# Kernel optimization log

Measured on AMD Instinct MI355X. Metric: run time of the kernel, lower is better.

The kernel has to match this reference:

```python
import jax, jax.numpy as jnp
import numpy as np

NEG = -1e9  # sentinel for suppressed / below-threshold scores
SCORE_THRESHOLD = 0.05
IOU_THRESHOLD = 0.5
MAX_DETECTIONS = 100


def _iou_one_vs_all(box, boxes):
    # box: (4,) in (x1, y1, x2, y2); boxes: (N, 4)
    ix1 = jnp.maximum(box[0], boxes[:, 0])
    iy1 = jnp.maximum(box[1], boxes[:, 1])
    ix2 = jnp.minimum(box[2], boxes[:, 2])
    iy2 = jnp.minimum(box[3], boxes[:, 3])
    inter = jnp.maximum(ix2 - ix1, 0.0) * jnp.maximum(iy2 - iy1, 0.0)
    a1 = (box[2] - box[0]) * (box[3] - box[1])
    a2 = (boxes[:, 2] - boxes[:, 0]) * (boxes[:, 3] - boxes[:, 1])
    return inter / jnp.maximum(a1 + a2 - inter, 1e-8)


def _nms_single_class(boxes, scores):
    # boxes: (N, 4), scores: (N,). Fixed-shape greedy NMS via scan.
    scores0 = jnp.where(scores > SCORE_THRESHOLD, scores, NEG)

    def step(s, _):
        best = jnp.argmax(s)
        bscore = s[best]
        bbox = boxes[best]
        iou = _iou_one_vs_all(bbox, boxes)
        # suppress overlapping boxes (incl. the selected one, IoU=1)
        s_next = jnp.where(iou > IOU_THRESHOLD, NEG, s)
        return s_next, (bscore, bbox)

    _, (keep_scores, keep_boxes) = jax.lax.scan(step, scores0, None, length=MAX_DETECTIONS)
    return keep_scores, keep_boxes  # (M,), (M, 4)


def _filter_one_image(boxes, classification):
    # boxes: (N, 4), classification: (N, C)
    C = classification.shape[1]
    cls_scores = classification.T  # (C, N)
    ks, kb = jax.vmap(lambda s: _nms_single_class(boxes, s))(cls_scores)  # (C, M), (C, M, 4)
    labels = jnp.broadcast_to(jnp.arange(C, dtype=jnp.int32)[:, None], ks.shape)
    scores_flat = ks.reshape(-1)          # (C*M,)
    boxes_flat = kb.reshape(-1, 4)        # (C*M, 4)
    labels_flat = labels.reshape(-1)      # (C*M,)
    top_scores, top_idx = jax.lax.top_k(scores_flat, MAX_DETECTIONS)
    top_boxes = boxes_flat[top_idx]
    top_labels = labels_flat[top_idx]
    valid = top_scores > SCORE_THRESHOLD
    out_scores = jnp.where(valid, top_scores, -1.0)
    out_boxes = jnp.where(valid[:, None], top_boxes, -1.0)
    out_labels = jnp.where(valid, top_labels, -1).astype(jnp.int32)
    return out_boxes, out_scores, out_labels


def setup_inputs() -> dict:
    key = jax.random.key(0)
    k1, k2, k3 = jax.random.split(key, 3)
    B, N, C = 2, 10000, 80
    xy = jax.random.uniform(k1, (B, N, 2), dtype=jnp.float32) * 900.0
    wh = jax.random.uniform(k2, (B, N, 2), dtype=jnp.float32) * 100.0 + 1.0
    boxes = jnp.concatenate([xy, xy + wh], axis=-1)  # valid (x1,y1,x2,y2)
    # raise to 4th power so most scores fall below the 0.05 threshold (realistic)
    classification = jax.random.uniform(k3, (B, N, C), dtype=jnp.float32) ** 4
    return {"boxes": boxes, "classification": classification}


@jax.jit
def reference(boxes, classification):
    # boxes: (B, N, 4), classification: (B, N, C)
    out_boxes, out_scores, out_labels = jax.vmap(_filter_one_image)(boxes, classification)
    return out_boxes, out_scores, out_labels
```

## Files before the change

kernel.cpp:

```cpp
#include <hip/hip_runtime.h>
#include <float.h>
#include <stdint.h>

#pragma clang fp contract(off)

#define NEGV   (-1e9f)
#define THRV   (0.05f)
#define MAXDET 100
#define NB     1152
#define BKBASE 31385
#define SLABSZ 1024
#define CHTGT  512
#define TKCAP  1024

__device__ __forceinline__ int bktOf(unsigned u) {
  int v = (int)(u >> 15) - BKBASE;
  return v < 0 ? 0 : (v > NB - 1 ? NB - 1 : v);
}

__device__ __forceinline__ bool killpair(
    float qx1, float qy1, float qx2, float qy2, float qa,
    float x1, float y1, float x2, float y2, float a)
{
  const float iw = fminf(qx2, x2) - fmaxf(qx1, x1);
  const float ih = fminf(qy2, y2) - fmaxf(qy1, y1);
  if (iw <= 0.f || ih <= 0.f) return false;
  const float inter = iw * ih;
  const float den = fmaxf((qa + a) - inter, 1e-8f);
  const float i2 = inter + inter;
  if (i2 > den * 1.00001f) return true;
  if (i2 < den * 0.99999f) return false;
  return (inter / den) > 0.5f;
}

template<int BT>
__device__ __forceinline__ int suffix_scan(int* hist, int* wtot,
                                           int tid, int lane, int wid) {
  int c0 = 0, c1 = 0, c2 = 0;
  if (tid < NB / 3) {
    c0 = hist[NB - 1 - 3 * tid];
    c1 = hist[NB - 2 - 3 * tid];
    c2 = hist[NB - 3 - 3 * tid];
  }
  const int tsum = c0 + c1 + c2;
  int inc = tsum;
#pragma unroll
  for (int off = 1; off < 64; off <<= 1) {
    const int u = __shfl_up(inc, off, 64);
    if (lane >= off) inc += u;
  }
  if (lane == 63) wtot[wid] = inc;
  __syncthreads();
  int wbase = 0, tot = 0;
#pragma unroll
  for (int w = 0; w < BT / 64; ++w) {
    const int v = wtot[w];
    if (w < wid) wbase += v;
    tot += v;
  }
  const int excl = wbase + inc - tsum;
  if (tid < NB / 3) {
    hist[NB - 1 - 3 * tid] = excl;
    hist[NB - 2 - 3 * tid] = excl + c0;
    hist[NB - 3 - 3 * tid] = excl + c0 + c1;
  }
  __syncthreads();
  return tot;
}

template<int BT>
__device__ int run_scan(
    const unsigned long long* kL, const unsigned long long* kG, bool useL,
    int cn, const float4* __restrict__ bb4,
    float4* kboxS, float* kscoreS, float* kareaS,
    unsigned long long* wkill, unsigned long long* killby,
    int tid, int lane, int wid)
{
#pragma clang fp contract(off)
  constexpr int NW = BT / 64;
  constexpr int CPW = 64 / NW;
  int nk = 0;
  for (int base = 0; base < cn && nk < MAXDET; base += 64) {
    const int nc = min(64, cn - base);
    const bool valid = lane < nc;
    const int p = base + lane;
    unsigned long long key = 0ull;
    if (valid) key = useL ? kL[p] : kG[p];
    const float score = __uint_as_float((unsigned)(key >> 32));
    const int idx = (int)(~(unsigned)key);
    float4 bx = make_float4(0.f, 0.f, 0.f, 0.f);
    if (valid) bx = bb4[idx];
    const float area = (bx.z - bx.x) * (bx.w - bx.y);

    bool kill = false;
    for (int e = wid; e < nk; e += NW) {
      const float4 q = kboxS[e];
      kill = kill || killpair(q.x, q.y, q.z, q.w, kareaS[e],
                              bx.x, bx.y, bx.z, bx.w, area);
    }
    {
      const unsigned long long bm = __ballot(valid && kill);
      if (lane == 0) wkill[wid] = bm;
    }
    {
      const int cb = wid * CPW;
#pragma unroll
      for (int jj = 0; jj < CPW; ++jj) {
        const int j = cb + jj;
        if (j < nc) {
          const float jx1 = __int_as_float(__builtin_amdgcn_readlane(__float_as_int(bx.x), j));
          const float jy1 = __int_as_float(__builtin_amdgcn_readlane(__float_as_int(bx.y), j));
          const float jx2 = __int_as_float(__builtin_amdgcn_readlane(__float_as_int(bx.z), j));
          const float jy2 = __int_as_float(__builtin_amdgcn_readlane(__float_as_int(bx.w), j));
          const float ja  = __int_as_float(__builtin_amdgcn_readlane(__float_as_int(area), j));
          const bool kij = valid && killpair(jx1, jy1, jx2, jy2, ja,
                                             bx.x, bx.y, bx.z, bx.w, area);
          const unsigned long long bm = __ballot(kij);
          if (lane == 0) killby[j] = bm;
        }
      }
    }
    __syncthreads();

    unsigned long long kmask = 0;
#pragma unroll
    for (int w = 0; w < NW; ++w) kmask |= wkill[w];
    unsigned long long alive = ~kmask;
    alive &= (nc >= 64) ? ~0ull : ((1ull << nc) - 1ull);
    const unsigned long long kb = killby[lane];
    for (int j = 0; j < 64; ++j) {
      if ((alive >> j) & 1ull) {
        const unsigned klo = (unsigned)__builtin_amdgcn_readlane((int)(unsigned)kb, j);
        const unsigned khi = (unsigned)__builtin_amdgcn_readlane((int)(unsigned)(kb >> 32), j);
        const unsigned long long km = ((unsigned long long)khi << 32) | klo;
        alive &= ~(km & ((~1ull) << j));
      }
    }
    if (wid == 0) {
      const int rank = (int)__popcll(alive & ((1ull << lane) - 1ull));
      if (((alive >> lane) & 1ull) && (nk + rank < MAXDET)) {
        kboxS[nk + rank] = bx;
        kscoreS[nk + rank] = score;
        kareaS[nk + rank] = area;
      }
    }
    nk += min((int)__popcll(alive), MAXDET - nk);
    __syncthreads();
  }
  return nk;
}

__global__ __launch_bounds__(256, 1) void transpose_kernel(
    const float* __restrict__ cls, float* __restrict__ clsT, int N, int C)
{
  __shared__ float tile[32][33];
  const int b = blockIdx.z;
  const int n0 = blockIdx.x * 32, c0 = blockIdx.y * 32;
  const int tx = threadIdx.x, ty = threadIdx.y;
#pragma unroll
  for (int r = ty; r < 32; r += 8) {
    const int n = n0 + r, c = c0 + tx;
    if (n < N && c < C) tile[r][tx] = cls[((size_t)b * N + n) * C + c];
  }
  __syncthreads();
#pragma unroll
  for (int r = ty; r < 32; r += 8) {
    const int c = c0 + r, n = n0 + tx;
    if (n < N && c < C) clsT[((size_t)b * C + c) * N + n] = tile[tx][r];
  }
}

template<int BT>
__global__ __launch_bounds__(BT, 1) void nms_kernel(
    const float* __restrict__ boxes, const float* __restrict__ clsT,
    unsigned long long* __restrict__ skg_all,
    float* __restrict__ ksc, float* __restrict__ kbx,
    int* __restrict__ ihist, int N, int C)
{
#pragma clang fp contract(off)
  const int bc = blockIdx.x;
  const int tid = threadIdx.x, lane = tid & 63, wid = tid >> 6;

  const float* ct = clsT + (size_t)bc * N;
  const float4* bb4 = (const float4*)(boxes + (size_t)(bc / C) * N * 4);
  unsigned long long* skg = skg_all + (size_t)bc * N;

  __shared__ unsigned long long slab[SLABSZ];
  __shared__ unsigned long long sorted[SLABSZ];
  __shared__ int hist[NB];
  __shared__ int wtot[BT / 64];
  __shared__ float4 kboxS[MAXDET];
  __shared__ float  kscoreS[MAXDET];
  __shared__ float  kareaS[MAXDET];
  __shared__ unsigned long long wkill[BT / 64];
  __shared__ unsigned long long killby[64];
  __shared__ int bkLoS;

  for (int i = tid; i < NB; i += BT) hist[i] = 0;
  if (tid == 0) bkLoS = -1;
  __syncthreads();
  for (int i = tid; i < N; i += BT) {
    const float s = ct[i];
    if (s > THRV) atomicAdd(&hist[bktOf(__float_as_uint(s))], 1);
  }
  __syncthreads();

  const int cn = suffix_scan<BT>(hist, wtot, tid, lane, wid);

  for (int bk = tid; bk < NB; bk += BT)
    if (hist[bk] >= CHTGT) atomicMax(&bkLoS, bk);
  __syncthreads();
  const int bkLo = bkLoS;
  const int chunkCnt = (bkLo >= 0) ? hist[bkLo] : cn;

  int nk = 0;
  bool slow = (chunkCnt > SLABSZ);
  if (!slow) {
    for (int i = tid; i < N; i += BT) {
      const float s = ct[i];
      if (s > THRV) {
        const unsigned u = __float_as_uint(s);
        const int bk = bktOf(u);
        if (bk > bkLo) {
          const int pos = atomicAdd(&hist[bk], 1);
          slab[pos] = ((unsigned long long)u << 32) | (unsigned)(~i);
        }
      }
    }
    __syncthreads();
    for (int e = tid; e < chunkCnt; e += BT) {
      const unsigned long long k = slab[e];
      int r = 0;
      for (int j = 0; j < chunkCnt; ++j) r += (slab[j] > k) ? 1 : 0;
      sorted[r] = k;
    }
    __syncthreads();
    nk = run_scan<BT>(sorted, skg, true, chunkCnt, bb4,
                      kboxS, kscoreS, kareaS, wkill, killby, tid, lane, wid);
    slow = (nk < MAXDET && chunkCnt < cn);
  }

  if (slow) {
    __syncthreads();
    for (int i = tid; i < NB; i += BT) hist[i] = 0;
    __syncthreads();
    for (int i = tid; i < N; i += BT) {
      const float s = ct[i];
      if (s > THRV) atomicAdd(&hist[bktOf(__float_as_uint(s))], 1);
    }
    __syncthreads();
    suffix_scan<BT>(hist, wtot, tid, lane, wid);
    for (int i = tid; i < N; i += BT) {
      const float s = ct[i];
      if (s > THRV) {
        const unsigned u = __float_as_uint(s);
        const int pos = atomicAdd(&hist[bktOf(u)], 1);
        skg[pos] = ((unsigned long long)u << 32) | (unsigned)(~i);
      }
    }
    __syncthreads();
    for (int bk = tid; bk < NB; bk += BT) {
      const int lo = (bk == NB - 1) ? 0 : hist[bk + 1];
      const int hi = hist[bk];
      for (int x = lo + 1; x < hi; ++x) {
        const unsigned long long v = skg[x];
        int y = x - 1;
        while (y >= lo && skg[y] < v) { skg[y + 1] = skg[y]; --y; }
        skg[y + 1] = v;
      }
    }
    __syncthreads();
    nk = run_scan<BT>(sorted, skg, false, cn, bb4,
                      kboxS, kscoreS, kareaS, wkill, killby, tid, lane, wid);
  }

  float* ko  = ksc + (size_t)bc * MAXDET;
  float* kbo = kbx + (size_t)bc * MAXDET * 4;
  int* ih = ihist + (size_t)(bc / C) * NB;
  for (int e = tid; e < MAXDET; e += BT) {
    if (e < nk) {
      const float4 q = kboxS[e];
      const float s = kscoreS[e];
      ko[e] = s;
      kbo[e * 4 + 0] = q.x; kbo[e * 4 + 1] = q.y;
      kbo[e * 4 + 2] = q.z; kbo[e * 4 + 3] = q.w;
      atomicAdd(&ih[bktOf(__float_as_uint(s))], 1);
    } else {
      ko[e] = NEGV;
      kbo[e * 4 + 0] = 0.f; kbo[e * 4 + 1] = 0.f;
      kbo[e * 4 + 2] = 0.f; kbo[e * 4 + 3] = 0.f;
    }
  }
}

template<int BT>
__global__ __launch_bounds__(BT, 1) void topk_kernel(
    const float* __restrict__ ksc, const float* __restrict__ kbx,
    const int* __restrict__ ihist, unsigned long long* __restrict__ gcand_all,
    float* __restrict__ out, int B, int C)
{
  const int b = blockIdx.x;
  const int tid = threadIdx.x, lane = tid & 63, wid = tid >> 6;
  const int T = C * MAXDET;
  const float* s0 = ksc + (size_t)b * T;
  unsigned long long* gc = gcand_all + (size_t)b * T;
  float* ob = out;
  float* os = out + (size_t)B * MAXDET * 4;
  float* ol = os + (size_t)B * MAXDET;

  __shared__ int hist[NB];
  __shared__ int wtot[BT / 64];
  __shared__ unsigned long long cand[TKCAP];
  __shared__ int tBs, cposS;

  for (int i = tid; i < NB; i += BT) hist[i] = ihist[(size_t)b * NB + i];
  if (tid == 0) { cposS = 0; tBs = 0; }
  __syncthreads();
  suffix_scan<BT>(hist, wtot, tid, lane, wid);
  for (int bk = tid; bk < NB; bk += BT)
    if (hist[bk] < MAXDET && (bk == 0 || hist[bk - 1] >= MAXDET)) tBs = bk;
  __syncthreads();
  const int t = tBs;
  for (int f = tid; f < T; f += BT) {
    const float s = s0[f];
    if (s > THRV) {
      const unsigned u = __float_as_uint(s);
      if (bktOf(u) >= t) {
        const int p = atomicAdd(&cposS, 1);
        const unsigned long long key =
            ((unsigned long long)u << 32) | (unsigned)(~f);
        if (p < TKCAP) cand[p] = key; else gc[p] = key;
      }
    }
  }
  __syncthreads();
  const int nc = cposS;
  const int nw = min(nc, MAXDET);
  for (int s2 = nw + tid; s2 < MAXDET; s2 += BT) {
    float* od = ob + ((size_t)b * MAXDET + s2) * 4;
    od[0] = -1.f; od[1] = -1.f; od[2] = -1.f; od[3] = -1.f;
    os[(size_t)b * MAXDET + s2] = -1.f;
    ol[(size_t)b * MAXDET + s2] = -1.f;
  }
  for (int e = tid; e < nc; e += BT) {
    const unsigned long long k = (e < TKCAP) ? cand[e] : gc[e];
    int rank = 0;
    for (int j = 0; j < nc; ++j) {
      const unsigned long long o = (j < TKCAP) ? cand[j] : gc[j];
      rank += (o > k) ? 1 : 0;
    }
    if (rank < MAXDET) {
      const int f = (int)(~(unsigned)k);
      const float sc = __uint_as_float((unsigned)(k >> 32));
      const float* bp = kbx + ((size_t)b * T + f) * 4;
      float* od = ob + ((size_t)b * MAXDET + rank) * 4;
      od[0] = bp[0]; od[1] = bp[1]; od[2] = bp[2]; od[3] = bp[3];
      os[(size_t)b * MAXDET + rank] = sc;
      ol[(size_t)b * MAXDET + rank] = (float)(f / MAXDET);
    }
  }
}

extern "C" void kernel_launch(void* const* d_in, const int* in_sizes, int n_in,
                              void* d_out, int out_size, void* d_ws, size_t ws_size,
                              hipStream_t stream) {
  const float* boxes = (const float*)d_in[0];
  const float* cls   = (const float*)d_in[1];
  const int B = out_size / (MAXDET * 6);
  const int N = in_sizes[0] / (B * 4);
  const int C = in_sizes[1] / (B * N);

  char* ws = (char*)d_ws;
  unsigned long long* skg = (unsigned long long*)ws;
  ws += (size_t)B * C * N * 8;
  unsigned long long* gcand = (unsigned long long*)ws;
  ws += (size_t)B * C * MAXDET * 8;
  float* clsT = (float*)ws; ws += (size_t)B * C * N * 4;
  float* kbx = (float*)ws;  ws += (size_t)B * C * MAXDET * 16;
  float* ksc = (float*)ws;  ws += (size_t)B * C * MAXDET * 4;
  int* ihist = (int*)ws;

  hipMemsetAsync(ihist, 0, (size_t)B * NB * 4, stream);
  transpose_kernel<<<dim3((N + 31) / 32, (C + 31) / 32, B), dim3(32, 8),
                     0, stream>>>(cls, clsT, N, C);
  nms_kernel<1024><<<dim3(B * C), dim3(1024), 0, stream>>>(
      boxes, clsT, skg, ksc, kbx, ihist, N, C);
  topk_kernel<1024><<<dim3(B), dim3(1024), 0, stream>>>(
      ksc, kbx, ihist, gcand, (float*)d_out, B, C);
}
```

Before: 159.6 us.

## Fuse threshold compaction and histogram into transpose sweep, replace slow path with selection

```diff
diff --git a/kernel.cpp b/kernel.cpp
--- a/kernel.cpp
+++ b/kernel.cpp
@@ -11,6 +11,7 @@
 #define BKBASE 31385
 #define SLABSZ 1024
 #define CHTGT  512
+#define PREB   256
 #define TKCAP  1024
 
 __device__ __forceinline__ int bktOf(unsigned u) {
@@ -69,12 +70,12 @@
 }
 
 template<int BT>
-__device__ int run_scan(
-    const unsigned long long* kL, const unsigned long long* kG, bool useL,
-    int cn, const float4* __restrict__ bb4,
-    float4* kboxS, float* kscoreS, float* kareaS,
-    unsigned long long* wkill, unsigned long long* killby,
-    int tid, int lane, int wid)
+__device__ int run_scan(const unsigned long long* keys, int cn,
+                        const float4* __restrict__ bb4,
+                        const float4* boxPre, int preN,
+                        float4* kboxS, float* kscoreS, float* kareaS,
+                        unsigned long long* wkill, unsigned long long* killby,
+                        int tid, int lane, int wid)
 {
 #pragma clang fp contract(off)
   constexpr int NW = BT / 64;
@@ -85,11 +86,11 @@
     const bool valid = lane < nc;
     const int p = base + lane;
     unsigned long long key = 0ull;
-    if (valid) key = useL ? kL[p] : kG[p];
+    if (valid) key = keys[p];
     const float score = __uint_as_float((unsigned)(key >> 32));
     const int idx = (int)(~(unsigned)key);
     float4 bx = make_float4(0.f, 0.f, 0.f, 0.f);
-    if (valid) bx = bb4[idx];
+    if (valid) bx = (p < preN) ? boxPre[p] : bb4[idx];
     const float area = (bx.z - bx.x) * (bx.w - bx.y);
 
     bool kill = false;
@@ -150,63 +151,130 @@
   return nk;
 }
 
-__global__ __launch_bounds__(256, 1) void transpose_kernel(
-    const float* __restrict__ cls, float* __restrict__ clsT, int N, int C)
+template<int BT>
+__device__ int selection_tail(const unsigned long long* __restrict__ cd,
+                              int cn, unsigned long long lastKey, int nk,
+                              const float4* __restrict__ bb4,
+                              float4* kboxS, float* kscoreS, float* kareaS,
+                              unsigned long long* redS, int* flagS,
+                              int tid, int lane, int wid)
+{
+#pragma clang fp contract(off)
+  while (nk < MAXDET) {
+    unsigned long long best = 0ull;
+    for (int i = tid; i < cn; i += BT) {
+      const unsigned long long k = cd[i];
+      if (k < lastKey && k > best) best = k;
+    }
+#pragma unroll
+    for (int off = 32; off >= 1; off >>= 1) {
+      const unsigned long long o = __shfl_xor(best, off, 64);
+      if (o > best) best = o;
+    }
+    if (lane == 0) redS[wid] = best;
+    if (tid == 0) *flagS = 0;
+    __syncthreads();
+    unsigned long long gbest = redS[0];
+#pragma unroll
+    for (int w = 1; w < BT / 64; ++w) if (redS[w] > gbest) gbest = redS[w];
+    if (gbest == 0ull) break;
+    const int idx = (int)(~(unsigned)gbest);
+    const float4 q = bb4[idx];
+    const float qa = (q.z - q.x) * (q.w - q.y);
+    bool kl = false;
+    for (int e = tid; e < nk; e += BT) {
+      const float4 kq = kboxS[e];
+      kl = kl || killpair(kq.x, kq.y, kq.z, kq.w, kareaS[e],
+                          q.x, q.y, q.z, q.w, qa);
+    }
+    if (kl) atomicOr(flagS, 1);
+    __syncthreads();
+    const bool killed = (*flagS != 0);
+    if (!killed) {
+      if (tid == 0) {
+        kboxS[nk] = q;
+        kscoreS[nk] = __uint_as_float((unsigned)(gbest >> 32));
+        kareaS[nk] = qa;
+      }
+      ++nk;
+    }
+    __syncthreads();
+    lastKey = gbest;
+  }
+  return nk;
+}
+
+__global__ __launch_bounds__(256, 1) void sweep_kernel(
+    const float* __restrict__ cls, unsigned long long* __restrict__ cand,
+    int* __restrict__ cnt, int* __restrict__ ghist, int N, int C)
 {
   __shared__ float tile[32][33];
   const int b = blockIdx.z;
   const int n0 = blockIdx.x * 32, c0 = blockIdx.y * 32;
   const int tx = threadIdx.x, ty = threadIdx.y;
-#pragma unroll
   for (int r = ty; r < 32; r += 8) {
     const int n = n0 + r, c = c0 + tx;
     if (n < N && c < C) tile[r][tx] = cls[((size_t)b * N + n) * C + c];
   }
   __syncthreads();
-#pragma unroll
-  for (int r = ty; r < 32; r += 8) {
-    const int c = c0 + r, n = n0 + tx;
-    if (n < N && c < C) clsT[((size_t)b * C + c) * N + n] = tile[tx][r];
+  const int t = ty * 32 + tx;
+  const int l = t & 31;
+  const int g = t >> 5;
+  const int lane = t & 63;
+#pragma unroll
+  for (int pass = 0; pass < 4; ++pass) {
+    const int ccol = pass * 8 + g;
+    const int c = c0 + ccol;
+    const int n = n0 + l;
+    const float s = tile[l][ccol];
+    const bool pred = (c < C) && (n < N) && (s > THRV);
+    const unsigned long long bal = __ballot(pred);
+    const unsigned hm = (unsigned)(bal >> (lane & 32));
+    const int npass = __popc(hm);
+    int base = 0;
+    if ((l == 0) && npass) base = atomicAdd(&cnt[b * C + c], npass);
+    base = __shfl(base, lane & 32, 64);
+    if (pred) {
+      const unsigned u = __float_as_uint(s);
+      const int rank = __popc(hm & ((1u << l) - 1u));
+      const size_t bcIdx = (size_t)(b * C + c);
+      cand[bcIdx * N + base + rank] =
+          ((unsigned long long)u << 32) | (unsigned)(~n);
+      atomicAdd(&ghist[bcIdx * NB + bktOf(u)], 1);
+    }
   }
 }
 
 template<int BT>
 __global__ __launch_bounds__(BT, 1) void nms_kernel(
-    const float* __restrict__ boxes, const float* __restrict__ clsT,
-    unsigned long long* __restrict__ skg_all,
-    float* __restrict__ ksc, float* __restrict__ kbx,
-    int* __restrict__ ihist, int N, int C)
+    const float* __restrict__ boxes,
+    const unsigned long long* __restrict__ cand,
+    const int* __restrict__ cnt, const int* __restrict__ ghist,
+    float* __restrict__ ksc, float* __restrict__ kbx, int N, int C)
 {
 #pragma clang fp contract(off)
   const int bc = blockIdx.x;
+  const int cn = cnt[bc];
   const int tid = threadIdx.x, lane = tid & 63, wid = tid >> 6;
-
-  const float* ct = clsT + (size_t)bc * N;
+  const unsigned long long* cd = cand + (size_t)bc * N;
   const float4* bb4 = (const float4*)(boxes + (size_t)(bc / C) * N * 4);
-  unsigned long long* skg = skg_all + (size_t)bc * N;
-
+
+  __shared__ int hist[NB];
+  __shared__ int wtot[BT / 64];
   __shared__ unsigned long long slab[SLABSZ];
   __shared__ unsigned long long sorted[SLABSZ];
-  __shared__ int hist[NB];
-  __shared__ int wtot[BT / 64];
+  __shared__ float4 boxPre[PREB];
   __shared__ float4 kboxS[MAXDET];
-  __shared__ float  kscoreS[MAXDET];
-  __shared__ float  kareaS[MAXDET];
-  __shared__ unsigned long long wkill[BT / 64];
-  __shared__ unsigned long long killby[64];
+  __shared__ float kscoreS[MAXDET], kareaS[MAXDET];
+  __shared__ unsigned long long wkill[BT / 64], killby[64];
+  __shared__ unsigned long long redS[BT / 64];
+  __shared__ int flagS;
   __shared__ int bkLoS;
 
-  for (int i = tid; i < NB; i += BT) hist[i] = 0;
+  for (int i = tid; i < NB; i += BT) hist[i] = ghist[(size_t)bc * NB + i];
   if (tid == 0) bkLoS = -1;
   __syncthreads();
-  for (int i = tid; i < N; i += BT) {
-    const float s = ct[i];
-    if (s > THRV) atomicAdd(&hist[bktOf(__float_as_uint(s))], 1);
-  }
-  __syncthreads();
-
-  const int cn = suffix_scan<BT>(hist, wtot, tid, lane, wid);
-
+  suffix_scan<BT>(hist, wtot, tid, lane, wid);
   for (int bk = tid; bk < NB; bk += BT)
     if (hist[bk] >= CHTGT) atomicMax(&bkLoS, bk);
   __syncthreads();
@@ -214,18 +282,11 @@
   const int chunkCnt = (bkLo >= 0) ? hist[bkLo] : cn;
 
   int nk = 0;
-  bool slow = (chunkCnt > SLABSZ);
-  if (!slow) {
-    for (int i = tid; i < N; i += BT) {
-      const float s = ct[i];
-      if (s > THRV) {
-        const unsigned u = __float_as_uint(s);
-        const int bk = bktOf(u);
-        if (bk > bkLo) {
-          const int pos = atomicAdd(&hist[bk], 1);
-          slab[pos] = ((unsigned long long)u << 32) | (unsigned)(~i);
-        }
-      }
+  if (chunkCnt <= SLABSZ) {
+    for (int i = tid; i < cn; i += BT) {
+      const unsigned long long k = cd[i];
+      const int bk = bktOf((unsigned)(k >> 32));
+      if (bk > bkLo) slab[atomicAdd(&hist[bk], 1)] = k;
     }
     __syncthreads();
     for (int e = tid; e < chunkCnt; e += BT) {
@@ -235,56 +296,30 @@
       sorted[r] = k;
     }
     __syncthreads();
-    nk = run_scan<BT>(sorted, skg, true, chunkCnt, bb4,
+    const int preN = min(chunkCnt, PREB);
+    for (int e = tid; e < preN; e += BT)
+      boxPre[e] = bb4[(int)(~(unsigned)sorted[e])];
+    __syncthreads();
+    nk = run_scan<BT>(sorted, chunkCnt, bb4, boxPre, preN,
                       kboxS, kscoreS, kareaS, wkill, killby, tid, lane, wid);
-    slow = (nk < MAXDET && chunkCnt < cn);
-  }
-
-  if (slow) {
-    __syncthreads();
-    for (int i = tid; i < NB; i += BT) hist[i] = 0;
-    __syncthreads();
-    for (int i = tid; i < N; i += BT) {
-      const float s = ct[i];
-      if (s > THRV) atomicAdd(&hist[bktOf(__float_as_uint(s))], 1);
-    }
-    __syncthreads();
-    suffix_scan<BT>(hist, wtot, tid, lane, wid);
-    for (int i = tid; i < N; i += BT) {
-      const float s = ct[i];
-      if (s > THRV) {
-        const unsigned u = __float_as_uint(s);
-        const int pos = atomicAdd(&hist[bktOf(u)], 1);
-        skg[pos] = ((unsigned long long)u << 32) | (unsigned)(~i);
-      }
-    }
-    __syncthreads();
-    for (int bk = tid; bk < NB; bk += BT) {
-      const int lo = (bk == NB - 1) ? 0 : hist[bk + 1];
-      const int hi = hist[bk];
-      for (int x = lo + 1; x < hi; ++x) {
-        const unsigned long long v = skg[x];
-        int y = x - 1;
-        while (y >= lo && skg[y] < v) { skg[y + 1] = skg[y]; --y; }
-        skg[y + 1] = v;
-      }
-    }
-    __syncthreads();
-    nk = run_scan<BT>(sorted, skg, false, cn, bb4,
-                      kboxS, kscoreS, kareaS, wkill, killby, tid, lane, wid);
+    if (nk < MAXDET && chunkCnt < cn)
+      nk = selection_tail<BT>(cd, cn, sorted[chunkCnt - 1], nk, bb4,
+                              kboxS, kscoreS, kareaS, redS, &flagS,
+                              tid, lane, wid);
+  } else {
+    nk = selection_tail<BT>(cd, cn, ~0ull, 0, bb4,
+                            kboxS, kscoreS, kareaS, redS, &flagS,
+                            tid, lane, wid);
   }
 
   float* ko  = ksc + (size_t)bc * MAXDET;
   float* kbo = kbx + (size_t)bc * MAXDET * 4;
-  int* ih = ihist + (size_t)(bc / C) * NB;
   for (int e = tid; e < MAXDET; e += BT) {
     if (e < nk) {
       const float4 q = kboxS[e];
-      const float s = kscoreS[e];
-      ko[e] = s;
+      ko[e] = kscoreS[e];
       kbo[e * 4 + 0] = q.x; kbo[e * 4 + 1] = q.y;
       kbo[e * 4 + 2] = q.z; kbo[e * 4 + 3] = q.w;
-      atomicAdd(&ih[bktOf(__float_as_uint(s))], 1);
     } else {
       ko[e] = NEGV;
       kbo[e * 4 + 0] = 0.f; kbo[e * 4 + 1] = 0.f;
@@ -296,7 +331,7 @@
 template<int BT>
 __global__ __launch_bounds__(BT, 1) void topk_kernel(
     const float* __restrict__ ksc, const float* __restrict__ kbx,
-    const int* __restrict__ ihist, unsigned long long* __restrict__ gcand_all,
+    unsigned long long* __restrict__ gcand_all,
     float* __restrict__ out, int B, int C)
 {
   const int b = blockIdx.x;
@@ -310,11 +345,16 @@
 
   __shared__ int hist[NB];
   __shared__ int wtot[BT / 64];
-  __shared__ unsigned long long cand[TKCAP];
+  __shared__ unsigned long long candS[TKCAP];
   __shared__ int tBs, cposS;
 
-  for (int i = tid; i < NB; i += BT) hist[i] = ihist[(size_t)b * NB + i];
+  for (int i = tid; i < NB; i += BT) hist[i] = 0;
   if (tid == 0) { cposS = 0; tBs = 0; }
+  __syncthreads();
+  for (int f = tid; f < T; f += BT) {
+    const float s = s0[f];
+    if (s > THRV) atomicAdd(&hist[bktOf(__float_as_uint(s))], 1);
+  }
   __syncthreads();
   suffix_scan<BT>(hist, wtot, tid, lane, wid);
   for (int bk = tid; bk < NB; bk += BT)
@@ -329,7 +369,7 @@
         const int p = atomicAdd(&cposS, 1);
         const unsigned long long key =
             ((unsigned long long)u << 32) | (unsigned)(~f);
-        if (p < TKCAP) cand[p] = key; else gc[p] = key;
+        if (p < TKCAP) candS[p] = key; else gc[p] = key;
       }
     }
   }
@@ -343,10 +383,10 @@
     ol[(size_t)b * MAXDET + s2] = -1.f;
   }
   for (int e = tid; e < nc; e += BT) {
-    const unsigned long long k = (e < TKCAP) ? cand[e] : gc[e];
+    const unsigned long long k = (e < TKCAP) ? candS[e] : gc[e];
     int rank = 0;
     for (int j = 0; j < nc; ++j) {
-      const unsigned long long o = (j < TKCAP) ? cand[j] : gc[j];
+      const unsigned long long o = (j < TKCAP) ? candS[j] : gc[j];
       rank += (o > k) ? 1 : 0;
     }
     if (rank < MAXDET) {
@@ -371,20 +411,20 @@
   const int C = in_sizes[1] / (B * N);
 
   char* ws = (char*)d_ws;
-  unsigned long long* skg = (unsigned long long*)ws;
+  unsigned long long* cand = (unsigned long long*)ws;
   ws += (size_t)B * C * N * 8;
+  float* kbx = (float*)ws;  ws += (size_t)B * C * MAXDET * 16;
+  float* ksc = (float*)ws;  ws += (size_t)B * C * MAXDET * 4;
   unsigned long long* gcand = (unsigned long long*)ws;
   ws += (size_t)B * C * MAXDET * 8;
-  float* clsT = (float*)ws; ws += (size_t)B * C * N * 4;
-  float* kbx = (float*)ws;  ws += (size_t)B * C * MAXDET * 16;
-  float* ksc = (float*)ws;  ws += (size_t)B * C * MAXDET * 4;
-  int* ihist = (int*)ws;
-
-  hipMemsetAsync(ihist, 0, (size_t)B * NB * 4, stream);
-  transpose_kernel<<<dim3((N + 31) / 32, (C + 31) / 32, B), dim3(32, 8),
-                     0, stream>>>(cls, clsT, N, C);
-  nms_kernel<1024><<<dim3(B * C), dim3(1024), 0, stream>>>(
-      boxes, clsT, skg, ksc, kbx, ihist, N, C);
-  topk_kernel<1024><<<dim3(B), dim3(1024), 0, stream>>>(
-      ksc, kbx, ihist, gcand, (float*)d_out, B, C);
-}
+  int* ghist = (int*)ws; ws += (size_t)B * C * NB * 4;
+  int* cnt = (int*)ws;
+
+  hipMemsetAsync(ghist, 0, (size_t)B * C * NB * 4 + (size_t)B * C * 4, stream);
+  sweep_kernel<<<dim3((N + 31) / 32, (C + 31) / 32, B), dim3(32, 8),
+                 0, stream>>>(cls, cand, cnt, ghist, N, C);
+  nms_kernel<512><<<dim3(B * C), dim3(512), 0, stream>>>(
+      boxes, cand, cnt, ghist, ksc, kbx, N, C);
+  topk_kernel<512><<<dim3(B), dim3(512), 0, stream>>>(
+      ksc, kbx, gcand, (float*)d_out, B, C);
+}
```

After: 230.3 us. +44.3%, slower.
